# Optimization experiments

Measured on AMD Instinct MI355X. Metric: run time of the kernel, lower is better.

The kernel has to match this reference:

```python
import jax, jax.numpy as jnp
import numpy as np
from itertools import product

# Static config
B, H, W, C = 16, 64, 64, 256
WIN = 8            # window size (square)
SHIFT = 4          # cyclic shift
NH = 8             # heads
HD = C // NH       # head dim
N = WIN * WIN      # tokens per window
HIDDEN = 1024


def _rel_pos_index():
    coords = np.stack(np.meshgrid(np.arange(WIN), np.arange(WIN), indexing='ij'))  # (2,w,w)
    flat = coords.reshape(2, -1)                                   # (2,N)
    rel = flat[:, :, None] - flat[:, None, :]                      # (2,N,N)
    rel = rel.transpose(1, 2, 0).astype(np.int64)
    rel[..., 0] += WIN - 1
    rel[..., 1] += WIN - 1
    rel[..., 0] *= 2 * WIN - 1
    return rel.sum(-1)                                             # (N,N)


def _shift_mask():
    # additive mask (nW, N, N) with -100 across shift boundaries (generate_mask)
    img = np.zeros((H, W), dtype=np.float32)
    slices = [(slice(0, -WIN), slice(-WIN, -SHIFT), slice(-SHIFT, None))] * 2
    cnt = 0
    for sx, sy in product(*slices):
        img[sx, sy] = cnt
        cnt += 1
    mw = img.reshape(H // WIN, WIN, W // WIN, WIN).transpose(0, 2, 1, 3).reshape(-1, N)  # (nW,N)
    diff = mw[:, None, :] - mw[:, :, None]
    return np.where(diff != 0, -100.0, 0.0).astype(np.float32)     # (nW,N,N)


REL_IDX = jnp.asarray(_rel_pos_index())
MASK = jnp.asarray(_shift_mask())


def _layernorm(x, scale, bias, eps=1e-5):
    mu = jnp.mean(x, axis=-1, keepdims=True)
    var = jnp.mean(jnp.square(x - mu), axis=-1, keepdims=True)
    return (x - mu) * jax.lax.rsqrt(var + eps) * scale + bias


def setup_inputs() -> dict:
    key = jax.random.key(0)
    ks = jax.random.split(key, 8)
    s = lambda fan_in: 1.0 / np.sqrt(fan_in)
    return {
        'x': jax.random.normal(ks[0], (B, H, W, C), jnp.float32),
        'ln1_scale': jnp.ones((C,), jnp.float32),
        'ln1_bias': jnp.zeros((C,), jnp.float32),
        'qkv_w': jax.random.normal(ks[1], (3 * C, C), jnp.float32) * s(C),
        'qkv_b': jnp.zeros((3 * C,), jnp.float32),
        'proj_w': jax.random.normal(ks[2], (C, C), jnp.float32) * s(C),
        'proj_b': jnp.zeros((C,), jnp.float32),
        'rel_bias': jax.random.normal(ks[3], ((2 * WIN - 1) ** 2, NH), jnp.float32) * 0.02,
        'ln2_scale': jnp.ones((C,), jnp.float32),
        'ln2_bias': jnp.zeros((C,), jnp.float32),
        'mlp_w1': jax.random.normal(ks[4], (HIDDEN, C), jnp.float32) * s(C),
        'mlp_b1': jnp.zeros((HIDDEN,), jnp.float32),
        'mlp_w2': jax.random.normal(ks[5], (C, HIDDEN), jnp.float32) * s(HIDDEN),
        'mlp_b2': jnp.zeros((C,), jnp.float32),
    }


def reference(x, ln1_scale, ln1_bias, qkv_w, qkv_b, proj_w, proj_b, rel_bias,
              ln2_scale, ln2_bias, mlp_w1, mlp_b1, mlp_w2, mlp_b2):
    nWh, nWw = H // WIN, W // WIN
    nW = nWh * nWw

    shortcut = x
    h = _layernorm(x, ln1_scale, ln1_bias)
    # cyclic shift
    h = jnp.roll(h, shift=(-SHIFT, -SHIFT), axis=(1, 2))
    # window partition -> (B*nW, N, C)
    h = h.reshape(B, nWh, WIN, nWw, WIN, C).transpose(0, 1, 3, 2, 4, 5).reshape(B * nW, N, C)

    # qkv
    qkv = h @ qkv_w.T + qkv_b                                # (B*nW, N, 3C)
    qkv = qkv.reshape(B * nW, N, 3, NH, HD)
    q, k, v = qkv[:, :, 0], qkv[:, :, 1], qkv[:, :, 2]       # (B*nW, N, NH, HD)

    scale = 1.0 / np.sqrt(HD)
    attn = jnp.einsum('bnhd,bmhd->bhnm', q * scale, k)       # (B*nW, NH, N, N)
    attn = attn + rel_bias[REL_IDX].transpose(2, 0, 1)[None]  # rel-pos bias (NH,N,N)
    attn = attn.reshape(B, nW, NH, N, N) + MASK[None, :, None]
    attn = jax.nn.softmax(attn.reshape(B * nW, NH, N, N), axis=-1)

    out = jnp.einsum('bhnm,bmhd->bnhd', attn, v).reshape(B * nW, N, C)
    out = out @ proj_w.T + proj_b

    # window reverse + reverse shift
    out = out.reshape(B, nWh, nWw, WIN, WIN, C).transpose(0, 1, 3, 2, 4, 5).reshape(B, H, W, C)
    out = jnp.roll(out, shift=(SHIFT, SHIFT), axis=(1, 2))

    x = shortcut + out
    # MLP
    h2 = _layernorm(x, ln2_scale, ln2_bias)
    h2 = jax.nn.gelu(h2 @ mlp_w1.T + mlp_b1, approximate=False) @ mlp_w2.T + mlp_b2
    return x + h2
```

## Files before the change

kernel.cpp:

```cpp
#include <hip/hip_runtime.h>
#include <hip/hip_bf16.h>
#include <math.h>

#define AS1 __attribute__((address_space(1)))
#define AS3 __attribute__((address_space(3)))

typedef __bf16  bf16x8 __attribute__((ext_vector_type(8)));
typedef float   f32x4  __attribute__((ext_vector_type(4)));
typedef __hip_bfloat16 bf16;

__device__ __forceinline__ void gload_lds16(const void* g, void* l) {
  __builtin_amdgcn_global_load_lds((const AS1 void*)g, (AS3 void*)l, 16, 0, 0);
}

__global__ __launch_bounds__(256) void k_conv_weights(
    const float* __restrict__ qkvw, const float* __restrict__ projw,
    const float* __restrict__ w1, const float* __restrict__ w2,
    bf16* __restrict__ dst)
{
  int i = blockIdx.x * 256 + threadIdx.x;
  float v;
  if (i < 196608)       v = qkvw[i];
  else if (i < 262144)  v = projw[i - 196608];
  else if (i < 524288)  v = w1[i - 262144];
  else                  v = w2[i - 524288];
  dst[i] = __float2bfloat16(v);
}

__global__ __launch_bounds__(256) void k_build_btab(
    const float* __restrict__ rel_bias, float* __restrict__ btab)
{
  int i = blockIdx.x * 256 + threadIdx.x;
  int h = i >> 12, r = i & 4095, n = r >> 6, m = r & 63;
  int idx = ((n >> 3) - (m >> 3) + 7) * 15 + ((n & 7) - (m & 7) + 7);
  btab[i] = rel_bias[idx * 8 + h];
}

__global__ __launch_bounds__(256) void k_ln1_window(
    const float* __restrict__ x, const float* __restrict__ sc,
    const float* __restrict__ bi, bf16* __restrict__ hout)
{
  int t = blockIdx.x * 4 + (threadIdx.x >> 6);
  int lane = threadIdx.x & 63;
  int win = t >> 6, nn = t & 63;
  int b = win >> 6, ww = win & 63;
  int ry = ((ww >> 3) << 3) + (nn >> 3);
  int rx = ((ww & 7) << 3) + (nn & 7);
  int sy = (ry + 4) & 63, sx = (rx + 4) & 63;
  const float* src = x + ((size_t)(((b << 6) + sy) << 6) + sx) * 256;
  f32x4 v = *(const f32x4*)(src + lane * 4);
  float s = v[0] + v[1] + v[2] + v[3];
  #pragma unroll
  for (int o = 1; o < 64; o <<= 1) s += __shfl_xor(s, o);
  float mu = s * (1.0f / 256.0f);
  float d0 = v[0]-mu, d1 = v[1]-mu, d2 = v[2]-mu, d3 = v[3]-mu;
  float q = d0*d0 + d1*d1 + d2*d2 + d3*d3;
  #pragma unroll
  for (int o = 1; o < 64; o <<= 1) q += __shfl_xor(q, o);
  float rstd = rsqrtf(q * (1.0f / 256.0f) + 1e-5f);
  int c = lane * 4;
  union { bf16 h[4]; uint2 u; } pk;
  pk.h[0] = __float2bfloat16(d0 * rstd * sc[c+0] + bi[c+0]);
  pk.h[1] = __float2bfloat16(d1 * rstd * sc[c+1] + bi[c+1]);
  pk.h[2] = __float2bfloat16(d2 * rstd * sc[c+2] + bi[c+2]);
  pk.h[3] = __float2bfloat16(d3 * rstd * sc[c+3] + bi[c+3]);
  *(uint2*)(hout + (size_t)t * 256 + c) = pk.u;
}

template<int EPI>
__global__ __launch_bounds__(256, 2) void k_pipe_ar(
    const bf16* __restrict__ A, const bf16* __restrict__ Bw,
    const float* __restrict__ bias,
    float* __restrict__ Cf, bf16* __restrict__ Cb,
    const float* __restrict__ resid,
    const float* __restrict__ ln2s, const float* __restrict__ ln2b,
    bf16* __restrict__ ln2out, int N)
{
  __shared__ __align__(16) char lds[65536 + 10240];

  const int tid = threadIdx.x;
  const int wid = tid >> 6;
  const int lane = tid & 63;
  const int l15 = lane & 15, lh = lane >> 4;
  const int rowBase = blockIdx.x * 128 + wid * 32;
  const int NC = N >> 5;
  char* scr = lds + 65536 + wid * 2560;

  auto stage = [&](int c) {
    char* dst = lds + (c & 3) * 16384;
    const char* srcB = (const char*)Bw + (size_t)c * 32 * 512;
    #pragma unroll
    for (int i = 0; i < 4; ++i) {
      int off = (i * 256 + tid) * 16;
      int r = off >> 9, cb = off & 511;
      int csw = cb ^ ((r & 7) << 4);
      gload_lds16(srcB + (size_t)r * 512 + csw, dst + off);
    }
  };

  bf16x8 af[2][8];
  {
    const bf16* a0 = A + (size_t)(rowBase + l15) * 256 + lh * 8;
    #pragma unroll
    for (int kk = 0; kk < 8; ++kk) {
      af[0][kk] = *(const bf16x8*)(a0 + kk * 32);
      af[1][kk] = *(const bf16x8*)(a0 + 4096 + kk * 32);
    }
  }

  auto remap = [&](int row) -> size_t {
    int win = row >> 6, nn = row & 63;
    int b = win >> 6, ww = win & 63;
    int ry = ((ww >> 3) << 3) + (nn >> 3);
    int rx = ((ww & 7) << 3) + (nn & 7);
    int fy = (ry + 4) & 63, fx = (rx + 4) & 63;
    return ((size_t)(((b << 6) + fy) << 6) + fx) * 256;
  };
  size_t ra0 = 0, ra1 = 0;
  size_t rbA, rbB;
  if (EPI == 2) {
    ra0 = remap(rowBase + l15);
    ra1 = remap(rowBase + 16 + l15);
    rbA = remap(rowBase + (lane >> 2));
    rbB = remap(rowBase + 16 + (lane >> 2));
  } else {
    rbA = (size_t)(rowBase + (lane >> 2)) * N;
    rbB = rbA + (size_t)16 * N;
  }

  const int cl = lh * 4;
  f32x4 bc0 = *(const f32x4*)(bias + cl);
  f32x4 bc1 = *(const f32x4*)(bias + cl + 16);
  f32x4 rc00, rc10, rc01, rc11;
  if (EPI == 2) {
    rc00 = *(const f32x4*)(resid + ra0 + cl);
    rc10 = *(const f32x4*)(resid + ra1 + cl);
    rc01 = *(const f32x4*)(resid + ra0 + cl + 16);
    rc11 = *(const f32x4*)(resid + ra1 + cl + 16);
  }
  stage(0); stage(1); stage(2);
  asm volatile("s_waitcnt vmcnt(8)" ::: "memory");
  __builtin_amdgcn_sched_barrier(0);

  float s0 = 0.f, q0 = 0.f, s1 = 0.f, q1 = 0.f;

  for (int c = 0; c < NC; ++c) {
    __builtin_amdgcn_s_barrier();
    __builtin_amdgcn_sched_barrier(0);

    f32x4 bn0, bn1, rn00, rn10, rn01, rn11;
    if (c + 1 < NC) {
      const int ncl = (c + 1) * 32 + cl;
      bn0 = *(const f32x4*)(bias + ncl);
      bn1 = *(const f32x4*)(bias + ncl + 16);
      if (EPI == 2) {
        rn00 = *(const f32x4*)(resid + ra0 + ncl);
        rn10 = *(const f32x4*)(resid + ra1 + ncl);
        rn01 = *(const f32x4*)(resid + ra0 + ncl + 16);
        rn11 = *(const f32x4*)(resid + ra1 + ncl + 16);
      }
    }
    if (c + 3 < NC) stage(c + 3);

    const char* buf = lds + (c & 3) * 16384;
    const int xr = (l15 & 7) << 4;
    const int base0 = l15 * 512;
    f32x4 a00 = (f32x4){0.f,0.f,0.f,0.f};
    f32x4 a10 = (f32x4){0.f,0.f,0.f,0.f};
    f32x4 a01 = (f32x4){0.f,0.f,0.f,0.f};
    f32x4 a11 = (f32x4){0.f,0.f,0.f,0.f};
    #pragma unroll
    for (int kk = 0; kk < 8; ++kk) {
      const int ko = (kk * 64 + lh * 16) ^ xr;
      bf16x8 b0 = *(const bf16x8*)(buf + base0 + ko);
      bf16x8 b1 = *(const bf16x8*)(buf + base0 + 8192 + ko);
      a00 = __builtin_amdgcn_mfma_f32_16x16x32_bf16(b0, af[0][kk], a00, 0, 0, 0);
      a10 = __builtin_amdgcn_mfma_f32_16x16x32_bf16(b0, af[1][kk], a10, 0, 0, 0);
      a01 = __builtin_amdgcn_mfma_f32_16x16x32_bf16(b1, af[0][kk], a01, 0, 0, 0);
      a11 = __builtin_amdgcn_mfma_f32_16x16x32_bf16(b1, af[1][kk], a11, 0, 0, 0);
    }

    const int cbs = c * 32 + (lane & 3) * 8;
    if (EPI == 0) {
      union { bf16 h[4]; uint2 u; } p00, p01, p10, p11;
      #pragma unroll
      for (int j = 0; j < 4; ++j) {
        p00.h[j] = __float2bfloat16(a00[j] + bc0[j]);
        p01.h[j] = __float2bfloat16(a01[j] + bc1[j]);
        p10.h[j] = __float2bfloat16(a10[j] + bc0[j]);
        p11.h[j] = __float2bfloat16(a11[j] + bc1[j]);
      }
      *(uint2*)(scr + l15 * 80 + lh * 8)            = p00.u;
      *(uint2*)(scr + l15 * 80 + 32 + lh * 8)       = p01.u;
      *(uint2*)(scr + (16 + l15) * 80 + lh * 8)     = p10.u;
      *(uint2*)(scr + (16 + l15) * 80 + 32 + lh * 8)= p11.u;
      uint4 r0 = *(const uint4*)(scr + (lane >> 2) * 80 + (lane & 3) * 16);
      uint4 r1 = *(const uint4*)(scr + (16 + (lane >> 2)) * 80 + (lane & 3) * 16);
      *(uint4*)(Cb + rbA + cbs) = r0;
      *(uint4*)(Cb + rbB + cbs) = r1;
    } else {
      const int colb0 = c * 32 + cl, colb1 = colb0 + 16;
      f32x4 o00, o10, o01, o11;
      #pragma unroll
      for (int j = 0; j < 4; ++j) {
        o00[j] = a00[j] + bc0[j] + rc00[j];
        o10[j] = a10[j] + bc0[j] + rc10[j];
        o01[j] = a01[j] + bc1[j] + rc01[j];
        o11[j] = a11[j] + bc1[j] + rc11[j];
      }
      *(f32x4*)(Cf + ra0 + colb0) = o00;
      *(f32x4*)(Cf + ra1 + colb0) = o10;
      *(f32x4*)(Cf + ra0 + colb1) = o01;
      *(f32x4*)(Cf + ra1 + colb1) = o11;
      #pragma unroll
      for (int j = 0; j < 4; ++j) {
        s0 += o00[j] + o01[j];  q0 += o00[j]*o00[j] + o01[j]*o01[j];
        s1 += o10[j] + o11[j];  q1 += o10[j]*o10[j] + o11[j]*o11[j];
      }
    }

    if (c + 1 < NC) {
      bc0 = bn0; bc1 = bn1;
      if (EPI == 2) { rc00 = rn00; rc10 = rn10; rc01 = rn01; rc11 = rn11; }
    }

    if (c + 1 < NC) {
      if (EPI == 2) {
        if (c == 0)            { asm volatile("s_waitcnt vmcnt(18)" ::: "memory"); }
        else if (c + 3 < NC)   { asm volatile("s_waitcnt vmcnt(28)" ::: "memory"); }
        else                   { asm volatile("s_waitcnt vmcnt(6)"  ::: "memory"); }
      } else {
        if (c == 0)            { asm volatile("s_waitcnt vmcnt(12)" ::: "memory"); }
        else if (c + 3 < NC)   { asm volatile("s_waitcnt vmcnt(16)" ::: "memory"); }
        else                   { asm volatile("s_waitcnt vmcnt(6)"  ::: "memory"); }
      }
      __builtin_amdgcn_sched_barrier(0);
    }
  }

  if (EPI == 2) {
    s0 += __shfl_xor(s0, 16); s0 += __shfl_xor(s0, 32);
    q0 += __shfl_xor(q0, 16); q0 += __shfl_xor(q0, 32);
    s1 += __shfl_xor(s1, 16); s1 += __shfl_xor(s1, 32);
    q1 += __shfl_xor(q1, 16); q1 += __shfl_xor(q1, 32);
    float mu0 = s0 * (1.0f / 256.0f);
    float rs0 = rsqrtf(q0 * (1.0f / 256.0f) - mu0 * mu0 + 1e-5f);
    float mu1 = s1 * (1.0f / 256.0f);
    float rs1 = rsqrtf(q1 * (1.0f / 256.0f) - mu1 * mu1 + 1e-5f);
    for (int c = 0; c < NC; ++c) {
      const int cb0 = c * 32 + cl, cb1 = cb0 + 16;
      f32x4 v00 = *(const f32x4*)(Cf + ra0 + cb0);
      f32x4 v01 = *(const f32x4*)(Cf + ra0 + cb1);
      f32x4 v10 = *(const f32x4*)(Cf + ra1 + cb0);
      f32x4 v11 = *(const f32x4*)(Cf + ra1 + cb1);
      f32x4 sa = *(const f32x4*)(ln2s + cb0);
      f32x4 sb = *(const f32x4*)(ln2s + cb1);
      f32x4 ba = *(const f32x4*)(ln2b + cb0);
      f32x4 bb = *(const f32x4*)(ln2b + cb1);
      union { bf16 h[4]; uint2 u; } p00, p01, p10, p11;
      #pragma unroll
      for (int j = 0; j < 4; ++j) {
        p00.h[j] = __float2bfloat16((v00[j] - mu0) * rs0 * sa[j] + ba[j]);
        p01.h[j] = __float2bfloat16((v01[j] - mu0) * rs0 * sb[j] + bb[j]);
        p10.h[j] = __float2bfloat16((v10[j] - mu1) * rs1 * sa[j] + ba[j]);
        p11.h[j] = __float2bfloat16((v11[j] - mu1) * rs1 * sb[j] + bb[j]);
      }
      *(uint2*)(scr + l15 * 80 + lh * 8)             = p00.u;
      *(uint2*)(scr + l15 * 80 + 32 + lh * 8)        = p01.u;
      *(uint2*)(scr + (16 + l15) * 80 + lh * 8)      = p10.u;
      *(uint2*)(scr + (16 + l15) * 80 + 32 + lh * 8) = p11.u;
      uint4 r0 = *(const uint4*)(scr + (lane >> 2) * 80 + (lane & 3) * 16);
      uint4 r1 = *(const uint4*)(scr + (16 + (lane >> 2)) * 80 + (lane & 3) * 16);
      const int cbs = c * 32 + (lane & 3) * 8;
      *(uint4*)(ln2out + rbA + cbs) = r0;
      *(uint4*)(ln2out + rbB + cbs) = r1;
    }
  }
}

__global__ __launch_bounds__(256, 2) void k_mlp(
    const bf16* __restrict__ A, const bf16* __restrict__ W1,
    const float* __restrict__ B1, const bf16* __restrict__ W2,
    const float* __restrict__ B2, float* __restrict__ X1)
{
  __shared__ __align__(16) char lds[79872];

  const int tid = threadIdx.x;
  const int wid = tid >> 6;
  const int lane = tid & 63;
  const int l15 = lane & 15, lh = lane >> 4;
  const int rowBase = blockIdx.x * 128 + wid * 32;
  char* scr   = lds + 65536 + wid * 2560;
  char* b1lds = lds + 75776;

  auto stage = [&](int c) {
    char* slot = lds + (c & 1) * 32768;
    const char* srcW1 = (const char*)W1 + (size_t)c * 32 * 512;
    #pragma unroll
    for (int i = 0; i < 4; ++i) {
      int off = (i * 256 + tid) * 16;
      int r = off >> 9, cb = off & 511;
      int csw = cb ^ ((r & 7) << 4);
      gload_lds16(srcW1 + (size_t)r * 512 + csw, slot + off);
    }
    #pragma unroll
    for (int i = 0; i < 4; ++i) {
      int off = (i * 256 + tid) * 16;
      int ch = off >> 12, row = (off >> 4) & 255;
      gload_lds16((const char*)W2 + (size_t)row * 2048 + (size_t)c * 64 + ch * 16,
                  slot + 16384 + off);
    }
  };

  gload_lds16((const char*)B1 + tid * 16, b1lds + tid * 16);
  bf16x8 af[2][8];
  {
    const bf16* a0 = A + (size_t)(rowBase + l15) * 256 + lh * 8;
    #pragma unroll
    for (int kk = 0; kk < 8; ++kk) {
      af[0][kk] = *(const bf16x8*)(a0 + kk * 32);
      af[1][kk] = *(const bf16x8*)(a0 + 4096 + kk * 32);
    }
  }
  stage(0);
  asm volatile("s_waitcnt vmcnt(0)" ::: "memory");
  __builtin_amdgcn_sched_barrier(0);

  f32x4 acc2[2][16];
  #pragma unroll
  for (int m = 0; m < 2; ++m)
    #pragma unroll
    for (int n = 0; n < 16; ++n) acc2[m][n] = (f32x4){0.f,0.f,0.f,0.f};

  for (int c = 0; c < 32; ++c) {
    __builtin_amdgcn_s_barrier();
    __builtin_amdgcn_sched_barrier(0);

    if (c + 1 < 32) stage(c + 1);

    const char* slot = lds + (c & 1) * 32768;
    const int xr = (l15 & 7) << 4;
    const int base0 = l15 * 512;
    f32x4 a00 = (f32x4){0.f,0.f,0.f,0.f};
    f32x4 a10 = (f32x4){0.f,0.f,0.f,0.f};
    f32x4 a01 = (f32x4){0.f,0.f,0.f,0.f};
    f32x4 a11 = (f32x4){0.f,0.f,0.f,0.f};
    #pragma unroll
    for (int kk = 0; kk < 8; ++kk) {
      const int ko = (kk * 64 + lh * 16) ^ xr;
      bf16x8 b0 = *(const bf16x8*)(slot + base0 + ko);
      bf16x8 b1 = *(const bf16x8*)(slot + base0 + 8192 + ko);
      a00 = __builtin_amdgcn_mfma_f32_16x16x32_bf16(b0, af[0][kk], a00, 0, 0, 0);
      a10 = __builtin_amdgcn_mfma_f32_16x16x32_bf16(b0, af[1][kk], a10, 0, 0, 0);
      a01 = __builtin_amdgcn_mfma_f32_16x16x32_bf16(b1, af[0][kk], a01, 0, 0, 0);
      a11 = __builtin_amdgcn_mfma_f32_16x16x32_bf16(b1, af[1][kk], a11, 0, 0, 0);
    }

    f32x4 bv0 = *(const f32x4*)(b1lds + c * 128 + lh * 16);
    f32x4 bv1 = *(const f32x4*)(b1lds + c * 128 + 64 + lh * 16);
    auto gelu = [](float v) -> bf16 {
      float w = fmaf(v * v, 0.1029434f, 2.3022083f);
      float e = __builtin_amdgcn_exp2f(-v * w);
      return __float2bfloat16(v * __builtin_amdgcn_rcpf(1.0f + e));
    };
    union { bf16 h[4]; uint2 u; } p00, p01, p10, p11;
    #pragma unroll
    for (int j = 0; j < 4; ++j) {
      p00.h[j] = gelu(a00[j] + bv0[j]);
      p01.h[j] = gelu(a01[j] + bv1[j]);
      p10.h[j] = gelu(a10[j] + bv0[j]);
      p11.h[j] = gelu(a11[j] + bv1[j]);
    }
    *(uint2*)(scr + l15 * 80 + lh * 8)             = p00.u;
    *(uint2*)(scr + l15 * 80 + 32 + lh * 8)        = p01.u;
    *(uint2*)(scr + (16 + l15) * 80 + lh * 8)      = p10.u;
    *(uint2*)(scr + (16 + l15) * 80 + 32 + lh * 8) = p11.u;
    bf16x8 actf0 = *(const bf16x8*)(scr + l15 * 80 + lh * 16);
    bf16x8 actf1 = *(const bf16x8*)(scr + (16 + l15) * 80 + lh * 16);

    const char* w2buf = slot + 16384;
    const int w2k = lh * 4096;
    #pragma unroll
    for (int n = 0; n < 16; ++n) {
      bf16x8 wf = *(const bf16x8*)(w2buf + w2k + (n * 16 + l15) * 16);
      acc2[0][n] = __builtin_amdgcn_mfma_f32_16x16x32_bf16(wf, actf0, acc2[0][n], 0, 0, 0);
      acc2[1][n] = __builtin_amdgcn_mfma_f32_16x16x32_bf16(wf, actf1, acc2[1][n], 0, 0, 0);
    }

    if (c + 1 < 32) {
      asm volatile("s_waitcnt vmcnt(0)" ::: "memory");
      __builtin_amdgcn_sched_barrier(0);
    }
  }

  #pragma unroll
  for (int m = 0; m < 2; ++m) {
    size_t rowAddr = (size_t)(rowBase + m * 16 + l15) * 256;
    #pragma unroll
    for (int n = 0; n < 16; ++n) {
      const int colb = n * 16 + lh * 4;
      const f32x4 b4 = *(const f32x4*)(B2 + colb);
      f32x4* p = (f32x4*)(X1 + rowAddr + colb);
      f32x4 cc = *p;
      #pragma unroll
      for (int j = 0; j < 4; ++j) cc[j] += acc2[m][n][j] + b4[j];
      *p = cc;
    }
  }
}

__global__ __launch_bounds__(256) void k_attn(
    const bf16* __restrict__ qkv, const float* __restrict__ btab,
    bf16* __restrict__ outp)
{
  __shared__ __align__(16) char smem[71680];
  float* sb = (float*)smem;
  const int tid = threadIdx.x, wid = tid >> 6, lane = tid & 63;
  const int l15 = lane & 15, lh = lane >> 4;
  const int h = blockIdx.x >> 8;
  const int win = ((blockIdx.x & 255) << 2) + wid;
  const int tb = win << 6;
  char* plw = smem + 16384 + wid * 9216;
  char* vtw = smem + 16384 + 36864 + wid * 4608;

  for (int i = tid; i < 4096; i += 256) sb[i] = btab[(h << 12) + i];
  __syncthreads();

  bf16x8 qf[4], kf[4];
  #pragma unroll
  for (int m = 0; m < 4; ++m) {
    size_t base = (size_t)(tb + m * 16 + l15) * 768 + h * 32 + lh * 8;
    qf[m] = *(const bf16x8*)(qkv + base);
    kf[m] = *(const bf16x8*)(qkv + base + 256);
  }
  f32x4 s[4][4];
  #pragma unroll
  for (int i = 0; i < 4; ++i)
    #pragma unroll
    for (int j = 0; j < 4; ++j) {
      s[i][j] = (f32x4){0.f,0.f,0.f,0.f};
      s[i][j] = __builtin_amdgcn_mfma_f32_16x16x32_bf16(qf[i], kf[j], s[i][j], 0, 0, 0);
    }

  #pragma unroll
  for (int it = 0; it < 32; ++it) {
    int idx = it * 64 + lane;
    int m = idx >> 5, d = idx & 31;
    bf16 vv = qkv[(size_t)(tb + m) * 768 + 512 + h * 32 + d];
    *(bf16*)(vtw + d * 144 + m * 2) = vv;
  }

  int ww = win & 63, wi = ww >> 3, wj = ww & 7;
  int labm[4];
  #pragma unroll
  for (int jf = 0; jf < 4; ++jf) {
    int m = jf * 16 + l15;
    int yy = wi * 8 + (m >> 3), xx = wj * 8 + (m & 7);
    labm[jf] = (yy < 56 ? 0 : (yy < 60 ? 1 : 2)) * 3 + (xx < 56 ? 0 : (xx < 60 ? 1 : 2));
  }
  float rsum[4][4];
  const float scale = 0.17677669529663687f;
  #pragma unroll
  for (int i = 0; i < 4; ++i) {
    #pragma unroll
    for (int j = 0; j < 4; ++j) {
      int n = i * 16 + lh * 4 + j;
      int yy = wi * 8 + (n >> 3), xx = wj * 8 + (n & 7);
      int labn = (yy < 56 ? 0 : (yy < 60 ? 1 : 2)) * 3 + (xx < 56 ? 0 : (xx < 60 ? 1 : 2));
      float vals[4]; float mx = -1e30f;
      #pragma unroll
      for (int jf = 0; jf < 4; ++jf) {
        int m = jf * 16 + l15;
        float v = s[i][jf][j] * scale + sb[(n << 6) + m];
        if (labn != labm[jf]) v -= 100.0f;
        vals[jf] = v; mx = fmaxf(mx, v);
      }
      #pragma unroll
      for (int o = 1; o < 16; o <<= 1) mx = fmaxf(mx, __shfl_xor(mx, o));
      float sum = 0.0f;
      #pragma unroll
      for (int jf = 0; jf < 4; ++jf) {
        float e = __expf(vals[jf] - mx);
        sum += e;
        *(bf16*)(plw + n * 144 + (jf * 16 + l15) * 2) = __float2bfloat16(e);
      }
      #pragma unroll
      for (int o = 1; o < 16; o <<= 1) sum += __shfl_xor(sum, o);
      rsum[i][j] = sum;
    }
  }
  __syncthreads();

  f32x4 o[4][2];
  #pragma unroll
  for (int i = 0; i < 4; ++i) { o[i][0] = (f32x4){0.f,0.f,0.f,0.f}; o[i][1] = (f32x4){0.f,0.f,0.f,0.f}; }
  #pragma unroll
  for (int kk = 0; kk < 2; ++kk) {
    bf16x8 pf[4], vf[2];
    #pragma unroll
    for (int i = 0; i < 4; ++i)
      pf[i] = *(const bf16x8*)(plw + (i * 16 + l15) * 144 + kk * 64 + lh * 16);
    #pragma unroll
    for (int df = 0; df < 2; ++df)
      vf[df] = *(const bf16x8*)(vtw + (df * 16 + l15) * 144 + kk * 64 + lh * 16);
    #pragma unroll
    for (int i = 0; i < 4; ++i)
      #pragma unroll
      for (int df = 0; df < 2; ++df)
        o[i][df] = __builtin_amdgcn_mfma_f32_16x16x32_bf16(pf[i], vf[df], o[i][df], 0, 0, 0);
  }
  #pragma unroll
  for (int i = 0; i < 4; ++i)
    #pragma unroll
    for (int df = 0; df < 2; ++df)
      #pragma unroll
      for (int j = 0; j < 4; ++j) {
        int n = i * 16 + lh * 4 + j;
        int d = df * 16 + l15;
        float v = o[i][df][j] / rsum[i][j];
        outp[(size_t)(tb + n) * 256 + h * 32 + d] = __float2bfloat16(v);
      }
}

extern "C" void kernel_launch(void* const* d_in, const int* in_sizes, int n_in,
                              void* d_out, int out_size, void* d_ws, size_t ws_size,
                              hipStream_t stream) {
  (void)in_sizes; (void)n_in; (void)out_size; (void)ws_size;
  const float* x      = (const float*)d_in[0];
  const float* ln1_s  = (const float*)d_in[1];
  const float* ln1_b  = (const float*)d_in[2];
  const float* qkv_w  = (const float*)d_in[3];
  const float* qkv_b  = (const float*)d_in[4];
  const float* proj_w = (const float*)d_in[5];
  const float* proj_b = (const float*)d_in[6];
  const float* rel_b  = (const float*)d_in[7];
  const float* ln2_s  = (const float*)d_in[8];
  const float* ln2_b  = (const float*)d_in[9];
  const float* w1     = (const float*)d_in[10];
  const float* b1     = (const float*)d_in[11];
  const float* w2     = (const float*)d_in[12];
  const float* b2     = (const float*)d_in[13];

  char* ws = (char*)d_ws;
  bf16*  wqkv  = (bf16*)(ws + 0);
  bf16*  wproj = wqkv + 196608;
  bf16*  wm1   = wqkv + 262144;
  bf16*  wm2   = wqkv + 524288;
  float* btab  = (float*)(ws + 1572864);
  bf16*  hbuf  = (bf16*)(ws + 2097152);
  bf16*  qkvb  = (bf16*)(ws + 35651584);
  bf16*  attnb = (bf16*)(ws + 136314880);
  bf16*  ln2buf = hbuf;
  float* x1    = (float*)d_out;

  k_conv_weights<<<3072, 256, 0, stream>>>(qkv_w, proj_w, w1, w2, wqkv);
  k_build_btab<<<128, 256, 0, stream>>>(rel_b, btab);
  k_ln1_window<<<16384, 256, 0, stream>>>(x, ln1_s, ln1_b, hbuf);
  k_pipe_ar<0><<<512, 256, 0, stream>>>(hbuf, wqkv, qkv_b, nullptr, qkvb, nullptr,
                                        nullptr, nullptr, nullptr, 768);
  k_attn<<<2048, 256, 0, stream>>>(qkvb, btab, attnb);
  k_pipe_ar<2><<<512, 256, 0, stream>>>(attnb, wproj, proj_b, x1, nullptr, x,
                                        ln2_s, ln2_b, ln2buf, 256);
  k_mlp<<<512, 256, 0, stream>>>(ln2buf, wm1, b1, wm2, b2, x1);
}
```

Measured before the change: 275.5 us.

## Software-pipeline MLP second GEMM one chunk behind first GEMM; vectorize V transpose loads

The fused MLP kernel now runs the W2 GEMM for chunk c-1 inside the W1 GEMM loop of chunk c, with W2 tiles staged into the other LDS slot, and drains the last chunk after the loop. This interleaves independent MFMA streams to hide latency and drops the serial GELU-then-GEMM2 dependency within each iteration. In the attention kernel, the scalar per-element V gather is replaced by four 16-byte row loads per lane, each scattered into the transposed LDS layout. The new schedule relies on LDS slot reuse staying correct across the barrier ordering, and it adds register pressure from carrying the activation fragments between iterations.

```diff
diff --git a/kernel.cpp b/kernel.cpp
--- a/kernel.cpp
+++ b/kernel.cpp
@@ -293,7 +293,7 @@
   char* scr   = lds + 65536 + wid * 2560;
   char* b1lds = lds + 75776;
 
-  auto stage = [&](int c) {
+  auto stage_w1 = [&](int c) {
     char* slot = lds + (c & 1) * 32768;
     const char* srcW1 = (const char*)W1 + (size_t)c * 32 * 512;
     #pragma unroll
@@ -303,12 +303,15 @@
       int csw = cb ^ ((r & 7) << 4);
       gload_lds16(srcW1 + (size_t)r * 512 + csw, slot + off);
     }
+  };
+  auto stage_w2 = [&](int c) {
+    char* dst = lds + ((c + 1) & 1) * 32768 + 16384;
     #pragma unroll
     for (int i = 0; i < 4; ++i) {
       int off = (i * 256 + tid) * 16;
       int ch = off >> 12, row = (off >> 4) & 255;
       gload_lds16((const char*)W2 + (size_t)row * 2048 + (size_t)c * 64 + ch * 16,
-                  slot + 16384 + off);
+                  dst + off);
     }
   };
 
@@ -322,7 +325,7 @@
       af[1][kk] = *(const bf16x8*)(a0 + 4096 + kk * 32);
     }
   }
-  stage(0);
+  stage_w1(0);
   asm volatile("s_waitcnt vmcnt(0)" ::: "memory");
   __builtin_amdgcn_sched_barrier(0);
 
@@ -331,29 +334,52 @@
   for (int m = 0; m < 2; ++m)
     #pragma unroll
     for (int n = 0; n < 16; ++n) acc2[m][n] = (f32x4){0.f,0.f,0.f,0.f};
+  bf16x8 actfA = {}, actfB = {};
 
   for (int c = 0; c < 32; ++c) {
     __builtin_amdgcn_s_barrier();
     __builtin_amdgcn_sched_barrier(0);
 
-    if (c + 1 < 32) stage(c + 1);
-
-    const char* slot = lds + (c & 1) * 32768;
+    if (c + 1 < 32) stage_w1(c + 1);
+    stage_w2(c);
+
+    const char* slot  = lds + (c & 1) * 32768;
+    const char* w2buf = slot + 16384;
     const int xr = (l15 & 7) << 4;
     const int base0 = l15 * 512;
+    const int w2k = lh * 4096;
     f32x4 a00 = (f32x4){0.f,0.f,0.f,0.f};
     f32x4 a10 = (f32x4){0.f,0.f,0.f,0.f};
     f32x4 a01 = (f32x4){0.f,0.f,0.f,0.f};
     f32x4 a11 = (f32x4){0.f,0.f,0.f,0.f};
-    #pragma unroll
-    for (int kk = 0; kk < 8; ++kk) {
-      const int ko = (kk * 64 + lh * 16) ^ xr;
-      bf16x8 b0 = *(const bf16x8*)(slot + base0 + ko);
-      bf16x8 b1 = *(const bf16x8*)(slot + base0 + 8192 + ko);
-      a00 = __builtin_amdgcn_mfma_f32_16x16x32_bf16(b0, af[0][kk], a00, 0, 0, 0);
-      a10 = __builtin_amdgcn_mfma_f32_16x16x32_bf16(b0, af[1][kk], a10, 0, 0, 0);
-      a01 = __builtin_amdgcn_mfma_f32_16x16x32_bf16(b1, af[0][kk], a01, 0, 0, 0);
-      a11 = __builtin_amdgcn_mfma_f32_16x16x32_bf16(b1, af[1][kk], a11, 0, 0, 0);
+    if (c > 0) {
+      #pragma unroll
+      for (int kk = 0; kk < 8; ++kk) {
+        const int ko = (kk * 64 + lh * 16) ^ xr;
+        bf16x8 b0 = *(const bf16x8*)(slot + base0 + ko);
+        bf16x8 b1 = *(const bf16x8*)(slot + base0 + 8192 + ko);
+        a00 = __builtin_amdgcn_mfma_f32_16x16x32_bf16(b0, af[0][kk], a00, 0, 0, 0);
+        a10 = __builtin_amdgcn_mfma_f32_16x16x32_bf16(b0, af[1][kk], a10, 0, 0, 0);
+        a01 = __builtin_amdgcn_mfma_f32_16x16x32_bf16(b1, af[0][kk], a01, 0, 0, 0);
+        a11 = __builtin_amdgcn_mfma_f32_16x16x32_bf16(b1, af[1][kk], a11, 0, 0, 0);
+        bf16x8 w0 = *(const bf16x8*)(w2buf + w2k + ((2*kk)   * 16 + l15) * 16);
+        bf16x8 w1f= *(const bf16x8*)(w2buf + w2k + ((2*kk+1) * 16 + l15) * 16);
+        acc2[0][2*kk]   = __builtin_amdgcn_mfma_f32_16x16x32_bf16(w0,  actfA, acc2[0][2*kk],   0, 0, 0);
+        acc2[1][2*kk]   = __builtin_amdgcn_mfma_f32_16x16x32_bf16(w0,  actfB, acc2[1][2*kk],   0, 0, 0);
+        acc2[0][2*kk+1] = __builtin_amdgcn_mfma_f32_16x16x32_bf16(w1f, actfA, acc2[0][2*kk+1], 0, 0, 0);
+        acc2[1][2*kk+1] = __builtin_amdgcn_mfma_f32_16x16x32_bf16(w1f, actfB, acc2[1][2*kk+1], 0, 0, 0);
+      }
+    } else {
+      #pragma unroll
+      for (int kk = 0; kk < 8; ++kk) {
+        const int ko = (kk * 64 + lh * 16) ^ xr;
+        bf16x8 b0 = *(const bf16x8*)(slot + base0 + ko);
+        bf16x8 b1 = *(const bf16x8*)(slot + base0 + 8192 + ko);
+        a00 = __builtin_amdgcn_mfma_f32_16x16x32_bf16(b0, af[0][kk], a00, 0, 0, 0);
+        a10 = __builtin_amdgcn_mfma_f32_16x16x32_bf16(b0, af[1][kk], a10, 0, 0, 0);
+        a01 = __builtin_amdgcn_mfma_f32_16x16x32_bf16(b1, af[0][kk], a01, 0, 0, 0);
+        a11 = __builtin_amdgcn_mfma_f32_16x16x32_bf16(b1, af[1][kk], a11, 0, 0, 0);
+      }
     }
 
     f32x4 bv0 = *(const f32x4*)(b1lds + c * 128 + lh * 16);
@@ -375,21 +401,22 @@
     *(uint2*)(scr + l15 * 80 + 32 + lh * 8)        = p01.u;
     *(uint2*)(scr + (16 + l15) * 80 + lh * 8)      = p10.u;
     *(uint2*)(scr + (16 + l15) * 80 + 32 + lh * 8) = p11.u;
-    bf16x8 actf0 = *(const bf16x8*)(scr + l15 * 80 + lh * 16);
-    bf16x8 actf1 = *(const bf16x8*)(scr + (16 + l15) * 80 + lh * 16);
-
-    const char* w2buf = slot + 16384;
+    actfA = *(const bf16x8*)(scr + l15 * 80 + lh * 16);
+    actfB = *(const bf16x8*)(scr + (16 + l15) * 80 + lh * 16);
+
+    asm volatile("s_waitcnt vmcnt(0)" ::: "memory");
+    __builtin_amdgcn_sched_barrier(0);
+  }
+
+  __builtin_amdgcn_s_barrier();
+  {
+    const char* w2buf = lds + 16384;
     const int w2k = lh * 4096;
     #pragma unroll
     for (int n = 0; n < 16; ++n) {
       bf16x8 wf = *(const bf16x8*)(w2buf + w2k + (n * 16 + l15) * 16);
-      acc2[0][n] = __builtin_amdgcn_mfma_f32_16x16x32_bf16(wf, actf0, acc2[0][n], 0, 0, 0);
-      acc2[1][n] = __builtin_amdgcn_mfma_f32_16x16x32_bf16(wf, actf1, acc2[1][n], 0, 0, 0);
-    }
-
-    if (c + 1 < 32) {
-      asm volatile("s_waitcnt vmcnt(0)" ::: "memory");
-      __builtin_amdgcn_sched_barrier(0);
+      acc2[0][n] = __builtin_amdgcn_mfma_f32_16x16x32_bf16(wf, actfA, acc2[0][n], 0, 0, 0);
+      acc2[1][n] = __builtin_amdgcn_mfma_f32_16x16x32_bf16(wf, actfB, acc2[1][n], 0, 0, 0);
     }
   }
 
@@ -442,12 +469,20 @@
       s[i][j] = __builtin_amdgcn_mfma_f32_16x16x32_bf16(qf[i], kf[j], s[i][j], 0, 0, 0);
     }
 
-  #pragma unroll
-  for (int it = 0; it < 32; ++it) {
-    int idx = it * 64 + lane;
-    int m = idx >> 5, d = idx & 31;
-    bf16 vv = qkv[(size_t)(tb + m) * 768 + 512 + h * 32 + d];
-    *(bf16*)(vtw + d * 144 + m * 2) = vv;
+  {
+    const bf16* vrow = qkv + (size_t)(tb + lane) * 768 + 512 + h * 32;
+    union { uint4 u; bf16 h8[8]; } v0, v1, v2, v3;
+    v0.u = *(const uint4*)(vrow);
+    v1.u = *(const uint4*)(vrow + 8);
+    v2.u = *(const uint4*)(vrow + 16);
+    v3.u = *(const uint4*)(vrow + 24);
+    #pragma unroll
+    for (int j = 0; j < 8; ++j) {
+      *(bf16*)(vtw + (j)      * 144 + lane * 2) = v0.h8[j];
+      *(bf16*)(vtw + (8 + j)  * 144 + lane * 2) = v1.h8[j];
+      *(bf16*)(vtw + (16 + j) * 144 + lane * 2) = v2.h8[j];
+      *(bf16*)(vtw + (24 + j) * 144 + lane * 2) = v3.h8[j];
+    }
   }
 
   int ww = win & 63, wi = ww >> 3, wj = ww & 7;
```

Result: no change. 276.4 us (+0.3%).
